# Optimization experiments

Measured on AMD Instinct MI355X. Metric: run time of the kernel, lower is better.

The kernel has to match this reference:

```python
import jax, jax.numpy as jnp
import numpy as np


def _rconv(x, w, b):
    # reflection-pad 1 then 3x3 valid conv (same spatial size), NCHW/OIHW
    xp = jnp.pad(x, ((0, 0), (0, 0), (1, 1), (1, 1)), mode='reflect')
    y = jax.lax.conv_general_dilated(
        xp, w, window_strides=(1, 1), padding='VALID',
        dimension_numbers=('NCHW', 'OIHW', 'NCHW'))
    return y + b[None, :, None, None]


def setup_inputs() -> dict:
    key = jax.random.key(0)
    ks = jax.random.split(key, 12)
    B, C, H, W = 4, 256, 64, 64
    IC = 128  # inter_channels
    s = lambda fan_in: 1.0 / np.sqrt(fan_in)
    return {
        'query_feat': jax.random.normal(ks[0], (B, C, H, W), jnp.float32),
        'key_feat': jax.random.normal(ks[1], (B, C, H, W), jnp.float32),
        # 1x1 conv projections (stored as [out, in])
        'w_theta': jax.random.normal(ks[2], (IC, C), jnp.float32) * s(C),
        'b_theta': jnp.zeros((IC,), jnp.float32),
        'w_phi': jax.random.normal(ks[3], (IC, C), jnp.float32) * s(C),
        'b_phi': jnp.zeros((IC,), jnp.float32),
        # post-correlation block: conv(1->32), residual(32), conv(32->1)
        'w_in': jax.random.normal(ks[4], (32, 1, 3, 3), jnp.float32) * s(9),
        'b_in': jnp.zeros((32,), jnp.float32),
        'w_r1': jax.random.normal(ks[5], (32, 32, 3, 3), jnp.float32) * s(32 * 9),
        'b_r1': jnp.zeros((32,), jnp.float32),
        'w_r2': jax.random.normal(ks[6], (32, 32, 3, 3), jnp.float32) * s(32 * 9),
        'b_r2': jnp.zeros((32,), jnp.float32),
        'w_out': jax.random.normal(ks[7], (1, 32, 3, 3), jnp.float32) * s(32 * 9),
        'b_out': jnp.zeros((1,), jnp.float32),
    }


def reference(query_feat, key_feat, w_theta, b_theta, w_phi, b_phi,
              w_in, b_in, w_r1, b_r1, w_r2, b_r2, w_out, b_out):
    B, C, H, W = query_feat.shape
    N = H * W
    # 1x1 conv projections, flattened to sequences
    theta = jnp.einsum('oc,bchw->bohw', w_theta, query_feat) + b_theta[None, :, None, None]
    phi = jnp.einsum('oc,bchw->bohw', w_phi, key_feat) + b_phi[None, :, None, None]
    theta = theta.reshape(B, -1, N).transpose(0, 2, 1)  # [B, N, IC]
    phi = phi.reshape(B, -1, N)                          # [B, IC, N]
    # correlation matrix [B, N, N] then max over key positions
    f = jnp.matmul(theta, phi)
    sim = jnp.max(f, axis=-1).reshape(B, 1, H, W)
    # post-correlation conv refinement
    h = _rconv(sim, w_in, b_in)                      # 1 -> 32
    r = jax.nn.relu(_rconv(h, w_r1, b_r1))           # residual block
    r = _rconv(r, w_r2, b_r2)
    h = h + r
    out = _rconv(h, w_out, b_out)                    # 32 -> 1
    return out
```

## Files before the change

### kernel.cpp

```cpp
#include <hip/hip_runtime.h>

#define B_ 4
#define C_ 256
#define HH 64
#define WW 64
#define N_ 4096
#define IC_ 128
#define JC_ 8

typedef __attribute__((ext_vector_type(8))) short bf16x8;
typedef __attribute__((ext_vector_type(4))) float f32x4;

__device__ __forceinline__ short f2bf(float f) {
    unsigned u = __builtin_bit_cast(unsigned, f);
    unsigned r = (u + 0x7FFFu + ((u >> 16) & 1u)) >> 16;
    return (short)r;
}

__device__ __forceinline__ int refl(int v) {
    return v < 0 ? -v : (v > 63 ? 126 - v : v);
}

__global__ __launch_bounds__(256) void k_cvt_w(const float* __restrict__ wt,
                                               const float* __restrict__ wp,
                                               short* __restrict__ wtb,
                                               short* __restrict__ wpb) {
    int i = blockIdx.x * 256 + threadIdx.x;
    wtb[i] = f2bf(wt[i]);
    wpb[i] = f2bf(wp[i]);
}

__global__ __launch_bounds__(256) void k_project(
    const float* __restrict__ qf, const float* __restrict__ kf,
    const short* __restrict__ wq, const short* __restrict__ wk,
    const float* __restrict__ bq, const float* __restrict__ bk,
    short* __restrict__ outq, short* __restrict__ outk) {
    int z = blockIdx.z;
    const float* x = z ? kf : qf;
    const short* wbf = z ? wk : wq;
    const float* bias = z ? bk : bq;
    short* outT = z ? outk : outq;

    int b = blockIdx.y;
    int n0 = blockIdx.x * 32;
    int t = threadIdx.x;
    int lane = t & 63, wv = t >> 6;
    int l15 = lane & 15, q4 = lane >> 4;
    const float* xb = x + (size_t)b * C_ * N_;

    __shared__ float xs[2][32][36];

    f32x4 acc[2][2];
#pragma unroll
    for (int rf = 0; rf < 2; rf++)
#pragma unroll
        for (int cfi = 0; cfi < 2; cfi++) acc[rf][cfi] = (f32x4){0.f, 0.f, 0.f, 0.f};

    int sr = t >> 3, sc = t & 7;
    *(f32x4*)(&xs[0][sr][sc * 4]) = *(const f32x4*)(xb + (size_t)sr * N_ + n0 + sc * 4);

    for (int ks = 0; ks < 8; ks++) {
        __syncthreads();
        int buf = ks & 1;
        if (ks < 7) {
            int cb = (ks + 1) * 32;
            *(f32x4*)(&xs[buf ^ 1][sr][sc * 4]) =
                *(const f32x4*)(xb + (size_t)(cb + sr) * N_ + n0 + sc * 4);
        }
        int cbase = ks * 32 + q4 * 8;
        bf16x8 a[2];
#pragma unroll
        for (int rf = 0; rf < 2; rf++)
#pragma unroll
            for (int j = 0; j < 8; j++) a[rf][j] = f2bf(xs[buf][q4 * 8 + j][rf * 16 + l15]);
#pragma unroll
        for (int cfi = 0; cfi < 2; cfi++) {
            int cf = wv * 2 + cfi;
            bf16x8 bfr = *(const bf16x8*)(wbf + (size_t)(cf * 16 + l15) * C_ + cbase);
#pragma unroll
            for (int rf = 0; rf < 2; rf++)
                acc[rf][cfi] = __builtin_amdgcn_mfma_f32_16x16x32_bf16(a[rf], bfr, acc[rf][cfi], 0, 0, 0);
        }
    }
#pragma unroll
    for (int cfi = 0; cfi < 2; cfi++) {
        int ic = (wv * 2 + cfi) * 16 + l15;
        float bv = bias[ic];
#pragma unroll
        for (int rf = 0; rf < 2; rf++) {
#pragma unroll
            for (int r = 0; r < 4; r++) {
                int n = n0 + rf * 16 + q4 * 4 + r;
                outT[((size_t)b * N_ + n) * IC_ + ic] = f2bf(acc[rf][cfi][r] + bv);
            }
        }
    }
}

__global__ __launch_bounds__(256, 4) void k_corr(const short* __restrict__ thetaT,
                                                 const short* __restrict__ phiT,
                                                 float* __restrict__ simp) {
    __shared__ short ph[2][64][136];

    int b = blockIdx.z, jc = blockIdx.y;
    int i0 = blockIdx.x * 128;
    int t = threadIdx.x;
    int lane = t & 63, w = t >> 6;
    int l15 = lane & 15, q4 = lane >> 4;

    const short* thb = thetaT + ((size_t)b * N_ + i0 + w * 32) * IC_;
    const short* phb = phiT + ((size_t)b * N_ + jc * (N_ / JC_)) * IC_;

    bf16x8 afr[2][4];
#pragma unroll
    for (int rf = 0; rf < 2; rf++)
#pragma unroll
        for (int ks = 0; ks < 4; ks++)
            afr[rf][ks] = *(const bf16x8*)(thb + (size_t)(rf * 16 + l15) * IC_ + ks * 32 + q4 * 8);

    int srow = t >> 4, sc8 = t & 15;
#pragma unroll
    for (int k = 0; k < 4; k++)
        *(bf16x8*)(&ph[0][srow + k * 16][sc8 * 8]) =
            *(const bf16x8*)(phb + (size_t)(srow + k * 16) * IC_ + sc8 * 8);

    f32x4 rmax[2];
#pragma unroll
    for (int rf = 0; rf < 2; rf++) rmax[rf] = (f32x4){-3.0e38f, -3.0e38f, -3.0e38f, -3.0e38f};

    const int NT = (N_ / JC_) / 64;
    for (int it = 0; it < NT; it++) {
        int buf = it & 1;
        __syncthreads();
        if (it < NT - 1) {
            int j0 = (it + 1) * 64;
#pragma unroll
            for (int k = 0; k < 4; k++)
                *(bf16x8*)(&ph[buf ^ 1][srow + k * 16][sc8 * 8]) =
                    *(const bf16x8*)(phb + (size_t)(j0 + srow + k * 16) * IC_ + sc8 * 8);
        }
#pragma unroll
        for (int jf = 0; jf < 4; jf++) {
            bf16x8 bfr[4];
#pragma unroll
            for (int ks = 0; ks < 4; ks++)
                bfr[ks] = *(const bf16x8*)(&ph[buf][jf * 16 + l15][ks * 32 + q4 * 8]);
#pragma unroll
            for (int rf = 0; rf < 2; rf++) {
                f32x4 a2 = (f32x4){0.f, 0.f, 0.f, 0.f};
#pragma unroll
                for (int ks = 0; ks < 4; ks++)
                    a2 = __builtin_amdgcn_mfma_f32_16x16x32_bf16(afr[rf][ks], bfr[ks], a2, 0, 0, 0);
#pragma unroll
                for (int r = 0; r < 4; r++) rmax[rf][r] = fmaxf(rmax[rf][r], a2[r]);
            }
        }
    }

#pragma unroll
    for (int rf = 0; rf < 2; rf++) {
#pragma unroll
        for (int r = 0; r < 4; r++) {
            float v = rmax[rf][r];
            v = fmaxf(v, __shfl_xor(v, 1));
            v = fmaxf(v, __shfl_xor(v, 2));
            v = fmaxf(v, __shfl_xor(v, 4));
            v = fmaxf(v, __shfl_xor(v, 8));
            rmax[rf][r] = v;
        }
    }
    if (l15 == 0) {
        float* sp = simp + ((size_t)(b * JC_ + jc)) * N_ + i0 + w * 32;
#pragma unroll
        for (int rf = 0; rf < 2; rf++)
#pragma unroll
            for (int r = 0; r < 4; r++) sp[rf * 16 + q4 * 4 + r] = rmax[rf][r];
    }
}

__global__ __launch_bounds__(256) void k_conv_in(const float* __restrict__ simp,
                                                 const float* __restrict__ w,
                                                 const float* __restrict__ bias,
                                                 float* __restrict__ h) {
    int y = blockIdx.x, b = blockIdx.y;
    int t = threadIdx.x;
    int oc = t >> 3, x8 = t & 7;
    __shared__ float srow[3][66];
    const float* sb = simp + (size_t)b * JC_ * N_;
    if (t < 192) {
        int r = t >> 6, x = t & 63;
        int idx = refl(y - 1 + r) * 64 + x;
        float v = -3.0e38f;
#pragma unroll
        for (int jc = 0; jc < JC_; jc++) v = fmaxf(v, sb[jc * N_ + idx]);
        srow[r][x + 1] = v;
    }
    if (t < 3) {
        int gy = refl(y - 1 + t);
        float vl = -3.0e38f, vr = -3.0e38f;
#pragma unroll
        for (int jc = 0; jc < JC_; jc++) {
            vl = fmaxf(vl, sb[jc * N_ + gy * 64 + 1]);
            vr = fmaxf(vr, sb[jc * N_ + gy * 64 + 62]);
        }
        srow[t][0] = vl;
        srow[t][65] = vr;
    }
    __syncthreads();

    float wr[9];
#pragma unroll
    for (int k = 0; k < 9; k++) wr[k] = w[oc * 9 + k];
    float bv = bias[oc];
    float acc[8];
#pragma unroll
    for (int xi = 0; xi < 8; xi++) acc[xi] = bv;
#pragma unroll
    for (int ky = 0; ky < 3; ky++)
#pragma unroll
        for (int kx = 0; kx < 3; kx++) {
            float wv2 = wr[ky * 3 + kx];
#pragma unroll
            for (int xi = 0; xi < 8; xi++) acc[xi] += wv2 * srow[ky][x8 * 8 + xi + kx];
        }
    float* op = h + (((size_t)b * 32 + oc) * 64 + y) * 64 + x8 * 8;
#pragma unroll
    for (int xi = 0; xi < 8; xi++) op[xi] = acc[xi];
}

template <bool RELU, bool ADD>
__global__ __launch_bounds__(256) void k_conv_r(const float* __restrict__ in,
                                                const float* __restrict__ w,
                                                const float* __restrict__ bias,
                                                float* __restrict__ out,
                                                const float* __restrict__ add) {
    int y = blockIdx.x, b = blockIdx.z;
    int oc0 = blockIdx.y * 16;
    int t = threadIdx.x;
    __shared__ float tile[32][3][68];
    __shared__ float wlds[32 * 16 * 12];

#pragma unroll
    for (int k = 0; k < 18; k++) {
        int id = t + k * 256;
        int ocl = id / 288;
        int rem = id - ocl * 288;
        int ic = rem / 9;
        int tap = rem - ic * 9;
        wlds[(ic * 16 + ocl) * 12 + tap] = w[(size_t)(oc0 + ocl) * 288 + rem];
    }

#pragma unroll
    for (int r = 0; r < 3; r++) {
        int gy = refl(y - 1 + r);
#pragma unroll
        for (int i = 0; i < 2; i++) {
            int idx = t + i * 256;
            int ic = idx >> 4, c4 = idx & 15;
            f32x4 v = *(const f32x4*)(in + (((size_t)b * 32 + ic) * 64 + gy) * 64 + c4 * 4);
#pragma unroll
            for (int s = 0; s < 4; s++) tile[ic][r][c4 * 4 + s + 1] = v[s];
        }
    }
    if (t < 96) {
        int ic = t / 3, r = t - ic * 3;
        int gy = refl(y - 1 + r);
        const float* row = in + (((size_t)b * 32 + ic) * 64 + gy) * 64;
        tile[ic][r][0] = row[1];
        tile[ic][r][65] = row[62];
    }
    __syncthreads();

    int ocl = t >> 4, x4 = (t & 15) * 4;
    float bv = bias[oc0 + ocl];
    float acc[4];
#pragma unroll
    for (int xi = 0; xi < 4; xi++) acc[xi] = bv;

#pragma unroll 2
    for (int ic = 0; ic < 32; ic++) {
        const float* wr = &wlds[(ic * 16 + ocl) * 12];
        f32x4 W0 = *(const f32x4*)(wr);
        f32x4 W1 = *(const f32x4*)(wr + 4);
        f32x4 W2 = *(const f32x4*)(wr + 8);
        float w0 = W0[0], w1 = W0[1], w2 = W0[2], w3 = W0[3];
        float w4 = W1[0], w5 = W1[1], w6 = W1[2], w7 = W1[3];
        float w8 = W2[0];
        float xr[3][8];
#pragma unroll
        for (int r = 0; r < 3; r++) {
            const float* rowp = &tile[ic][r][x4];
            f32x4 A = *(const f32x4*)(rowp);
            f32x4 Bv = *(const f32x4*)(rowp + 4);
            xr[r][0] = A[0]; xr[r][1] = A[1]; xr[r][2] = A[2]; xr[r][3] = A[3];
            xr[r][4] = Bv[0]; xr[r][5] = Bv[1]; xr[r][6] = Bv[2]; xr[r][7] = Bv[3];
        }
#pragma unroll
        for (int xi = 0; xi < 4; xi++) {
            acc[xi] += w0 * xr[0][xi] + w1 * xr[0][xi + 1] + w2 * xr[0][xi + 2] +
                       w3 * xr[1][xi] + w4 * xr[1][xi + 1] + w5 * xr[1][xi + 2] +
                       w6 * xr[2][xi] + w7 * xr[2][xi + 1] + w8 * xr[2][xi + 2];
        }
    }
    size_t off = (((size_t)b * 32 + oc0 + ocl) * 64 + y) * 64 + x4;
#pragma unroll
    for (int xi = 0; xi < 4; xi++) {
        float v = acc[xi];
        if (RELU) v = fmaxf(v, 0.f);
        if (ADD) v += add[off + xi];
        out[off + xi] = v;
    }
}

__global__ __launch_bounds__(256) void k_conv_out(const float* __restrict__ hb,
                                                  const float* __restrict__ w,
                                                  const float* __restrict__ bias,
                                                  float* __restrict__ outp) {
    int y = blockIdx.x, b = blockIdx.y;
    int t = threadIdx.x;
    int x = t & 63, g = t >> 6;
    __shared__ float red[4][64];
    __shared__ float wl[288];
    for (int k = t; k < 288; k += 256) wl[k] = w[k];
    __syncthreads();
    float acc = 0.f;
#pragma unroll
    for (int i = 0; i < 8; i++) {
        int ic = g * 8 + i;
        const float* wp = wl + ic * 9;
#pragma unroll
        for (int ky = 0; ky < 3; ky++) {
            int gy = refl(y + ky - 1);
            const float* row = hb + (((size_t)b * 32 + ic) * 64 + gy) * 64;
#pragma unroll
            for (int kx = 0; kx < 3; kx++) {
                int gx = refl(x + kx - 1);
                acc += wp[ky * 3 + kx] * row[gx];
            }
        }
    }
    red[g][x] = acc;
    __syncthreads();
    if (t < 64) {
        outp[((size_t)b * 64 + y) * 64 + x] =
            bias[0] + red[0][t] + red[1][t] + red[2][t] + red[3][t];
    }
}

extern "C" void kernel_launch(void* const* d_in, const int* in_sizes, int n_in,
                              void* d_out, int out_size, void* d_ws, size_t ws_size,
                              hipStream_t stream) {
    const float* q = (const float*)d_in[0];
    const float* kf = (const float*)d_in[1];
    const float* w_theta = (const float*)d_in[2];
    const float* b_theta = (const float*)d_in[3];
    const float* w_phi = (const float*)d_in[4];
    const float* b_phi = (const float*)d_in[5];
    const float* w_in = (const float*)d_in[6];
    const float* b_in = (const float*)d_in[7];
    const float* w_r1 = (const float*)d_in[8];
    const float* b_r1 = (const float*)d_in[9];
    const float* w_r2 = (const float*)d_in[10];
    const float* b_r2 = (const float*)d_in[11];
    const float* w_out = (const float*)d_in[12];
    const float* b_out = (const float*)d_in[13];
    float* out = (float*)d_out;

    char* ws = (char*)d_ws;
    short* thetaT = (short*)(ws);
    short* phiT = (short*)(ws + 4194304);
    short* wthb = (short*)(ws + 8388608);
    short* wphb = (short*)(ws + 8454144);
    float* simp = (float*)(ws + 8519680);
    float* h = (float*)(ws);
    float* r = (float*)(ws + 2097152);

    k_cvt_w<<<128, 256, 0, stream>>>(w_theta, w_phi, wthb, wphb);
    k_project<<<dim3(128, 4, 2), 256, 0, stream>>>(q, kf, wthb, wphb, b_theta, b_phi,
                                                   thetaT, phiT);
    k_corr<<<dim3(32, JC_, 4), 256, 0, stream>>>(thetaT, phiT, simp);
    k_conv_in<<<dim3(64, 4), 256, 0, stream>>>(simp, w_in, b_in, h);
    k_conv_r<true, false><<<dim3(64, 2, 4), 256, 0, stream>>>(h, w_r1, b_r1, r, nullptr);
    k_conv_r<false, true><<<dim3(64, 2, 4), 256, 0, stream>>>(r, w_r2, b_r2, h, h);
    k_conv_out<<<dim3(64, 4), 256, 0, stream>>>(h, w_out, b_out, out);
}
```

Baseline: 165.8 us.

## Fuse input conv and first residual conv into one kernel with halo recompute

Merges the 1->32 input conv and the first 32->32 ReLU conv into a single kernel. Each block recomputes three rows of h (with reflection) from five rows of the reduced similarity map and keeps them in shared memory, then runs the 32->32 conv directly from LDS. This removes one launch and the global round trip of h for the first residual conv. In exchange it recomputes neighbouring h rows, uses a grid of 256 blocks instead of 512, and needs a larger LDS footprint per block.

Result: slower. 174.6 us (+5.3%).

```diff
diff --git a/kernel.cpp b/kernel.cpp
--- a/kernel.cpp
+++ b/kernel.cpp
@@ -178,54 +178,113 @@
     }
 }
 
-__global__ __launch_bounds__(256) void k_conv_in(const float* __restrict__ simp,
-                                                 const float* __restrict__ w,
-                                                 const float* __restrict__ bias,
-                                                 float* __restrict__ h) {
+__global__ __launch_bounds__(256) void k_conv_ir(const float* __restrict__ simp,
+                                                 const float* __restrict__ w_in,
+                                                 const float* __restrict__ b_in,
+                                                 const float* __restrict__ w_r1,
+                                                 const float* __restrict__ b_r1,
+                                                 float* __restrict__ h,
+                                                 float* __restrict__ r) {
     int y = blockIdx.x, b = blockIdx.y;
     int t = threadIdx.x;
+    __shared__ float srow[5][66];
+    __shared__ float hs[3][32][66];
+    __shared__ float wlds[32 * 32 * 12];
+
+    for (int idx = t; idx < 9216; idx += 256) {
+        int oc = idx / 288, rem = idx - oc * 288;
+        int ic = rem / 9, tap = rem - ic * 9;
+        wlds[(ic * 32 + oc) * 12 + tap] = w_r1[idx];
+    }
+    int ybase = y - 2;
+    if (ybase < 0) ybase = 0;
+    if (ybase > 59) ybase = 59;
+    const float* sb = simp + (size_t)b * JC_ * N_;
+    for (int idx = t; idx < 320; idx += 256) {
+        int i = idx >> 6, x = idx & 63;
+        int row = ybase + i;
+        float v = -3.0e38f;
+#pragma unroll
+        for (int p = 0; p < JC_; p++) v = fmaxf(v, sb[p * N_ + row * 64 + x]);
+        srow[i][x + 1] = v;
+    }
+    if (t < 10) {
+        int i = t >> 1, side = t & 1;
+        int row = ybase + i;
+        int x = side ? 62 : 1;
+        float v = -3.0e38f;
+#pragma unroll
+        for (int p = 0; p < JC_; p++) v = fmaxf(v, sb[p * N_ + row * 64 + x]);
+        srow[i][side ? 65 : 0] = v;
+    }
+    __syncthreads();
+
     int oc = t >> 3, x8 = t & 7;
-    __shared__ float srow[3][66];
-    const float* sb = simp + (size_t)b * JC_ * N_;
-    if (t < 192) {
-        int r = t >> 6, x = t & 63;
-        int idx = refl(y - 1 + r) * 64 + x;
-        float v = -3.0e38f;
-#pragma unroll
-        for (int jc = 0; jc < JC_; jc++) v = fmaxf(v, sb[jc * N_ + idx]);
-        srow[r][x + 1] = v;
-    }
-    if (t < 3) {
-        int gy = refl(y - 1 + t);
-        float vl = -3.0e38f, vr = -3.0e38f;
-#pragma unroll
-        for (int jc = 0; jc < JC_; jc++) {
-            vl = fmaxf(vl, sb[jc * N_ + gy * 64 + 1]);
-            vr = fmaxf(vr, sb[jc * N_ + gy * 64 + 62]);
-        }
-        srow[t][0] = vl;
-        srow[t][65] = vr;
+    float wi[9];
+#pragma unroll
+    for (int k = 0; k < 9; k++) wi[k] = w_in[oc * 9 + k];
+    float bvi = b_in[oc];
+#pragma unroll
+    for (int rr = 0; rr < 3; rr++) {
+        int gy = refl(y - 1 + rr);
+        float acc[8];
+#pragma unroll
+        for (int xi = 0; xi < 8; xi++) acc[xi] = bvi;
+#pragma unroll
+        for (int ky = 0; ky < 3; ky++) {
+            int s = refl(gy - 1 + ky) - ybase;
+#pragma unroll
+            for (int kx = 0; kx < 3; kx++) {
+                float wv = wi[ky * 3 + kx];
+#pragma unroll
+                for (int xi = 0; xi < 8; xi++) acc[xi] += wv * srow[s][x8 * 8 + xi + kx];
+            }
+        }
+#pragma unroll
+        for (int xi = 0; xi < 8; xi++) hs[rr][oc][x8 * 8 + xi + 1] = acc[xi];
+        if (x8 == 0) hs[rr][oc][0] = acc[1];
+        if (x8 == 7) hs[rr][oc][65] = acc[6];
     }
     __syncthreads();
 
-    float wr[9];
-#pragma unroll
-    for (int k = 0; k < 9; k++) wr[k] = w[oc * 9 + k];
-    float bv = bias[oc];
+    for (int idx = t; idx < 2048; idx += 256) {
+        int o = idx >> 6, x = idx & 63;
+        h[(((size_t)b * 32 + o) * 64 + y) * 64 + x] = hs[1][o][x + 1];
+    }
+
+    float bv = b_r1[oc];
     float acc[8];
 #pragma unroll
     for (int xi = 0; xi < 8; xi++) acc[xi] = bv;
-#pragma unroll
-    for (int ky = 0; ky < 3; ky++)
-#pragma unroll
-        for (int kx = 0; kx < 3; kx++) {
-            float wv2 = wr[ky * 3 + kx];
-#pragma unroll
-            for (int xi = 0; xi < 8; xi++) acc[xi] += wv2 * srow[ky][x8 * 8 + xi + kx];
-        }
-    float* op = h + (((size_t)b * 32 + oc) * 64 + y) * 64 + x8 * 8;
-#pragma unroll
-    for (int xi = 0; xi < 8; xi++) op[xi] = acc[xi];
+    for (int ic = 0; ic < 32; ic++) {
+        const float* wr = &wlds[(ic * 32 + oc) * 12];
+        f32x4 W0 = *(const f32x4*)(wr);
+        f32x4 W1 = *(const f32x4*)(wr + 4);
+        f32x4 W2 = *(const f32x4*)(wr + 8);
+        float w0 = W0[0], w1 = W0[1], w2 = W0[2], w3 = W0[3];
+        float w4 = W1[0], w5 = W1[1], w6 = W1[2], w7 = W1[3];
+        float w8 = W2[0];
+        float xr[3][12];
+#pragma unroll
+        for (int rr = 0; rr < 3; rr++) {
+            const float* rowp = &hs[rr][ic][x8 * 8];
+            f32x4 A = *(const f32x4*)(rowp);
+            f32x4 Bv = *(const f32x4*)(rowp + 4);
+            f32x4 Cv = *(const f32x4*)(rowp + 8);
+            xr[rr][0] = A[0]; xr[rr][1] = A[1]; xr[rr][2] = A[2]; xr[rr][3] = A[3];
+            xr[rr][4] = Bv[0]; xr[rr][5] = Bv[1]; xr[rr][6] = Bv[2]; xr[rr][7] = Bv[3];
+            xr[rr][8] = Cv[0]; xr[rr][9] = Cv[1]; xr[rr][10] = Cv[2]; xr[rr][11] = Cv[3];
+        }
+#pragma unroll
+        for (int xi = 0; xi < 8; xi++) {
+            acc[xi] += w0 * xr[0][xi] + w1 * xr[0][xi + 1] + w2 * xr[0][xi + 2] +
+                       w3 * xr[1][xi] + w4 * xr[1][xi + 1] + w5 * xr[1][xi + 2] +
+                       w6 * xr[2][xi] + w7 * xr[2][xi + 1] + w8 * xr[2][xi + 2];
+        }
+    }
+    float* rp = r + (((size_t)b * 32 + oc) * 64 + y) * 64 + x8 * 8;
+#pragma unroll
+    for (int xi = 0; xi < 8; xi++) rp[xi] = fmaxf(acc[xi], 0.f);
 }
 
 template <bool RELU, bool ADD>
@@ -379,8 +438,7 @@
     k_project<<<dim3(128, 4, 2), 256, 0, stream>>>(q, kf, wthb, wphb, b_theta, b_phi,
                                                    thetaT, phiT);
     k_corr<<<dim3(32, JC_, 4), 256, 0, stream>>>(thetaT, phiT, simp);
-    k_conv_in<<<dim3(64, 4), 256, 0, stream>>>(simp, w_in, b_in, h);
-    k_conv_r<true, false><<<dim3(64, 2, 4), 256, 0, stream>>>(h, w_r1, b_r1, r, nullptr);
+    k_conv_ir<<<dim3(64, 4), 256, 0, stream>>>(simp, w_in, b_in, w_r1, b_r1, h, r);
     k_conv_r<false, true><<<dim3(64, 2, 4), 256, 0, stream>>>(r, w_r2, b_r2, h, h);
     k_conv_out<<<dim3(64, 4), 256, 0, stream>>>(h, w_out, b_out, out);
 }
```
